# Kernel tuning notes

Measured on AMD Instinct MI355X. Metric: run time of the kernel, lower is better.

The kernel has to match this reference:

```python
import jax, jax.numpy as jnp
import numpy as np

NUM_HEADS = 16

def setup_inputs() -> dict:
    key = jax.random.key(0)
    k1, k2, k3, k4, k5 = jax.random.split(key, 5)
    B, N, C = 4, 2048, 1024
    N2, Cy = 1024, 768
    x = jax.random.normal(k1, (B, N, C), dtype=jnp.float32)
    y = jax.random.normal(k2, (B, N2, Cy), dtype=jnp.float32)
    pad_mask = jax.random.randint(k3, (B, N), 0, 2).astype(jnp.bool_)
    # Linear weights (torch convention: out = inp @ W.T), scaled ~ fan-in init
    Wq = jax.random.normal(k4, (C, C), dtype=jnp.float32) * (C ** -0.5)
    Wkv = jax.random.normal(k5, (2 * C, Cy), dtype=jnp.float32) * (Cy ** -0.5)
    return {"x": x, "y": y, "pad_mask": pad_mask, "Wq": Wq, "Wkv": Wkv}


def reference(x, y, pad_mask, Wq, Wkv):
    B, N, C = x.shape
    N2 = y.shape[1]
    H = NUM_HEADS
    d = C // H
    scale = d ** -0.5
    # q: [B, H, N, d]
    q = (x @ Wq.T).reshape(B, N, H, d).transpose(0, 2, 1, 3)
    # kv: [B, N2, 2, H, d] -> k, v each [B, H, N2, d]
    kv = (y @ Wkv.T).reshape(B, N2, 2, H, d).transpose(2, 0, 3, 1, 4)
    k, v = kv[0], kv[1]
    # scores: [B, H, N, N2]
    attn = jnp.einsum("bhnd,bhmd->bhnm", q * scale, k)
    # pad_mask is indexed by the QUERY axis and broadcast over keys (faithful
    # to the original einops.repeat 'B Q -> B H Q L'). False -> -1e9.
    attn = jnp.where(pad_mask[:, None, :, None], attn, jnp.float32(-1e9))
    attn = jax.nn.softmax(attn, axis=-1)
    out = jnp.einsum("bhnm,bhmd->bhnd", attn, v)  # [B, H, N, d]
    return out.transpose(0, 2, 1, 3).reshape(B, N, C)
```

## Files before the change

### kernel.cpp

```cpp
#include <hip/hip_runtime.h>

typedef unsigned short u16;
typedef unsigned int u32;
typedef __attribute__((ext_vector_type(8))) __bf16 bf16x8;
typedef __attribute__((ext_vector_type(4))) float f32x4;

__device__ __forceinline__ u16 f2bf(float f) {
  unsigned u = __float_as_uint(f);
  u += 0x7FFFu + ((u >> 16) & 1u);
  return (u16)(u >> 16);
}

__device__ __forceinline__ float fast_exp2(float x) { return __builtin_amdgcn_exp2f(x); }
__device__ __forceinline__ float fast_rcp(float x) { return __builtin_amdgcn_rcpf(x); }

__global__ void cvt_all(const float* __restrict__ x, const float* __restrict__ Wq,
                        const float* __restrict__ y, const float* __restrict__ Wkv,
                        const int* __restrict__ mask,
                        u16* __restrict__ Xb, u16* __restrict__ Wqb,
                        u16* __restrict__ Yb, u16* __restrict__ Wkvb) {
  int i = blockIdx.x * 256 + threadIdx.x;
  const float4* src;
  u16* dst;
  int j;
  float sc;
  if (i < 2097152) {
    j = i; src = (const float4*)x; dst = Xb;
    sc = (mask[i >> 8] != 0) ? 1.0f : 0.0f;
  } else if (i < 2359296) {
    j = i - 2097152; src = (const float4*)Wq; dst = Wqb;
    sc = 0.18033688f;
  } else if (i < 3145728) {
    j = i - 2359296; src = (const float4*)y; dst = Yb;
    sc = 1.0f;
  } else {
    j = i - 3145728; src = (const float4*)Wkv; dst = Wkvb;
    sc = 1.0f;
  }
  float4 v = src[j];
  ushort4 o;
  o.x = f2bf(v.x * sc);
  o.y = f2bf(v.y * sc);
  o.z = f2bf(v.z * sc);
  o.w = f2bf(v.w * sc);
  ((ushort4*)dst)[j] = o;
}

__global__ __launch_bounds__(256) void gemm_dual(
    const u16* __restrict__ Aq, const u16* __restrict__ Bq, u16* __restrict__ Cq,
    const u16* __restrict__ Akv, const u16* __restrict__ Bkv, u16* __restrict__ Ckv) {
  __shared__ __align__(16) u16 sA[2 * 128 * 32];
  __shared__ __align__(16) u16 sB[2 * 128 * 32];
  const int t = threadIdx.x;
  const int wave = t >> 6;
  const int lane = t & 63;
  const int wm = (wave >> 1) * 64;
  const int wn = (wave & 1) * 64;
  const int fr = lane & 15;
  const int quad = lane >> 4;
  const int fk = quad * 8;
  const int sr = lane >> 2;
  const int sc = (lane & 3) * 8;

  const u16 *A, *B;
  u16* C;
  int N, K, bx, by;
  const int blk = blockIdx.x;
  if (blk < 512) {
    A = Aq; B = Bq; C = Cq; N = 1024; K = 1024;
    by = blk >> 6; bx = blk & 63;
  } else {
    A = Akv; B = Bkv; C = Ckv; N = 2048; K = 768;
    const int id = blk - 512;
    by = id >> 5; bx = id & 31;
  }

  f32x4 acc[4][4];
  const f32x4 z4 = {0.f, 0.f, 0.f, 0.f};
#pragma unroll
  for (int i = 0; i < 4; ++i)
#pragma unroll
    for (int j = 0; j < 4; ++j) acc[i][j] = z4;

  const u16* Abase = A + (size_t)bx * 128 * K;
  const u16* Bbase = B + (size_t)by * 128 * K;

  auto stage = [&](int k0, u16* dA, u16* dB) {
#pragma unroll
    for (int q = 0; q < 2; ++q) {
      const int chunk = wave * 2 + q;
      const int row = chunk * 16 + sr;
      __builtin_amdgcn_global_load_lds(
          (__attribute__((address_space(1))) void*)(Abase + (size_t)row * K + k0 + sc),
          (__attribute__((address_space(3))) void*)(dA + chunk * 512), 16, 0, 0);
      __builtin_amdgcn_global_load_lds(
          (__attribute__((address_space(1))) void*)(Bbase + (size_t)row * K + k0 + sc),
          (__attribute__((address_space(3))) void*)(dB + chunk * 512), 16, 0, 0);
    }
  };

  stage(0, sA, sB);
  __syncthreads();

  int it = 0;
  for (int k0 = 0; k0 < K; k0 += 32, ++it) {
    u16* cA = sA + (it & 1) * 4096;
    u16* cB = sB + (it & 1) * 4096;
    if (k0 + 32 < K) stage(k0 + 32, sA + ((it + 1) & 1) * 4096, sB + ((it + 1) & 1) * 4096);

    bf16x8 af[4], bfv[4];
#pragma unroll
    for (int i = 0; i < 4; ++i)
      af[i] = *(const bf16x8*)(cA + (wm + i * 16 + fr) * 32 + fk);
#pragma unroll
    for (int j = 0; j < 4; ++j)
      bfv[j] = *(const bf16x8*)(cB + (wn + j * 16 + fr) * 32 + fk);
#pragma unroll
    for (int i = 0; i < 4; ++i)
#pragma unroll
      for (int j = 0; j < 4; ++j)
        acc[i][j] = __builtin_amdgcn_mfma_f32_16x16x32_bf16(af[i], bfv[j], acc[i][j], 0, 0, 0);

    if (k0 + 32 < K) __syncthreads();
  }

#pragma unroll
  for (int i = 0; i < 4; ++i)
#pragma unroll
    for (int j = 0; j < 4; ++j)
#pragma unroll
      for (int r = 0; r < 4; ++r) {
        const int row = bx * 128 + wm + i * 16 + quad * 4 + r;
        const int col = by * 128 + wn + j * 16 + fr;
        C[(size_t)row * N + col] = f2bf(acc[i][j][r]);
      }
}

__global__ void transpose_v(const u16* __restrict__ KV, u16* __restrict__ Vt) {
  __shared__ u16 tile[64][66];
  const int t = threadIdx.x;
  const int rb = blockIdx.x * 64;
  const int h = blockIdx.y;
#pragma unroll
  for (int i = 0; i < 16; ++i) {
    int idx = i * 256 + t;
    int r = idx >> 6, c = idx & 63;
    tile[r][c] = KV[(size_t)(rb + r) * 2048 + 1024 + h * 64 + c];
  }
  __syncthreads();
  const int b = blockIdx.x >> 4;
  const int n2b = (blockIdx.x & 15) * 64;
#pragma unroll
  for (int i = 0; i < 16; ++i) {
    int idx = i * 256 + t;
    int dd = idx >> 6, n2 = idx & 63;
    int cperm = (n2 & 32) | (((n2 >> 2) & 3) << 3) | (((n2 >> 4) & 1) << 2) | (n2 & 3);
    Vt[(size_t)((b * 16 + h) * 64 + dd) * 1024 + n2b + cperm] = tile[n2][dd];
  }
}

__global__ __launch_bounds__(256, 2) void attn_kernel(
    const u16* __restrict__ Q, const u16* __restrict__ KV,
    const u16* __restrict__ Vt, float* __restrict__ Out) {
  __shared__ __align__(16) u16 sK[2 * 128 * 64];
  __shared__ __align__(16) u16 sV[2 * 64 * 128];
  __shared__ float red[4][2][4][16];

  const int t = threadIdx.x;
  const int wave = t >> 6;
  const int lane = t & 63;
  const int g = blockIdx.x & 63;
  const int qt = blockIdx.x >> 6;
  const int b = g >> 4;
  const int h = g & 15;
  const int q0 = qt * 128;
  const int fr = lane & 15;
  const int quad = lane >> 4;
  const int l3 = lane >> 3, l7 = lane & 7;
  const int l4 = lane >> 4, l15 = lane & 15;

  const u16* qbase = Q + (size_t)(b * 2048 + q0 + wave * 16 + fr) * 1024 + h * 64 + quad * 8;
  bf16x8 qa[2][2];
  qa[0][0] = *(const bf16x8*)(qbase);
  qa[0][1] = *(const bf16x8*)(qbase + 32);
  qa[1][0] = *(const bf16x8*)(qbase + (size_t)64 * 1024);
  qa[1][1] = *(const bf16x8*)(qbase + (size_t)64 * 1024 + 32);

  const int kq = (l7 ^ l3) * 8;
  auto stage = [&](int kcn, u16* dK, u16* dV) {
#pragma unroll
    for (int i = 0; i < 4; ++i) {
      const int j = wave * 4 + i;
      const u16* ksrc = KV + (size_t)(b * 1024 + kcn * 128 + 8 * j + l3) * 2048 + h * 64 + kq;
      __builtin_amdgcn_global_load_lds(
          (__attribute__((address_space(1))) void*)ksrc,
          (__attribute__((address_space(3))) void*)(dK + j * 512), 16, 0, 0);
      const int vq = (l15 ^ ((i & 1) * 4 + l4)) * 8;
      const u16* vsrc = Vt + (size_t)((b * 16 + h) * 64 + 4 * j + l4) * 1024 + kcn * 128 + vq;
      __builtin_amdgcn_global_load_lds(
          (__attribute__((address_space(1))) void*)vsrc,
          (__attribute__((address_space(3))) void*)(dV + j * 512), 16, 0, 0);
    }
  };

  stage(0, sK, sV);
  __syncthreads();

  const f32x4 z4 = {0.f, 0.f, 0.f, 0.f};
  f32x4 o[2][4];
  float l_run[2] = {0.f, 0.f};
#pragma unroll
  for (int hh = 0; hh < 2; ++hh)
#pragma unroll
    for (int nt = 0; nt < 4; ++nt) o[hh][nt] = z4;

  const int f7 = fr & 7;
  const int ck0 = (quad ^ f7) * 8;
  const int ck1 = ((quad ^ 4) ^ f7) * 8;

  for (int kc = 0; kc < 8; ++kc) {
    const u16* sKc = sK + (kc & 1) * 8192;
    const u16* sVc = sV + (kc & 1) * 8192;
    if (kc < 7) stage(kc + 1, sK + ((kc + 1) & 1) * 8192, sV + ((kc + 1) & 1) * 8192);

#pragma unroll
    for (int ks = 0; ks < 4; ++ks) {
      f32x4 s0[2], s1[2];
      {
        const u16* kb = sKc + ((2 * ks) * 16 + fr) * 64;
        bf16x8 k0 = *(const bf16x8*)(kb + ck0);
        bf16x8 k1 = *(const bf16x8*)(kb + ck1);
        s0[0] = __builtin_amdgcn_mfma_f32_16x16x32_bf16(k0, qa[0][0], z4, 0, 0, 0);
        s0[0] = __builtin_amdgcn_mfma_f32_16x16x32_bf16(k1, qa[0][1], s0[0], 0, 0, 0);
        s0[1] = __builtin_amdgcn_mfma_f32_16x16x32_bf16(k0, qa[1][0], z4, 0, 0, 0);
        s0[1] = __builtin_amdgcn_mfma_f32_16x16x32_bf16(k1, qa[1][1], s0[1], 0, 0, 0);
      }
      {
        const u16* kb = sKc + ((2 * ks + 1) * 16 + fr) * 64;
        bf16x8 k0 = *(const bf16x8*)(kb + ck0);
        bf16x8 k1 = *(const bf16x8*)(kb + ck1);
        s1[0] = __builtin_amdgcn_mfma_f32_16x16x32_bf16(k0, qa[0][0], z4, 0, 0, 0);
        s1[0] = __builtin_amdgcn_mfma_f32_16x16x32_bf16(k1, qa[0][1], s1[0], 0, 0, 0);
        s1[1] = __builtin_amdgcn_mfma_f32_16x16x32_bf16(k0, qa[1][0], z4, 0, 0, 0);
        s1[1] = __builtin_amdgcn_mfma_f32_16x16x32_bf16(k1, qa[1][1], s1[1], 0, 0, 0);
      }

      bf16x8 pa[2];
#pragma unroll
      for (int hh = 0; hh < 2; ++hh) {
        f32x4& a = (hh == 0) ? s0[0] : s0[1];
        f32x4& bb = (hh == 0) ? s1[0] : s1[1];
        float l = 0.f;
#pragma unroll
        for (int r = 0; r < 4; ++r) {
          float p0 = fast_exp2(a[r]); a[r] = p0; l += p0;
          float p1 = fast_exp2(bb[r]); bb[r] = p1; l += p1;
        }
        l_run[hh] += l;
        bf16x8 pv;
        pv[0] = (__bf16)a[0];  pv[1] = (__bf16)a[1];
        pv[2] = (__bf16)a[2];  pv[3] = (__bf16)a[3];
        pv[4] = (__bf16)bb[0]; pv[5] = (__bf16)bb[1];
        pv[6] = (__bf16)bb[2]; pv[7] = (__bf16)bb[3];
        pa[hh] = pv;
      }

#pragma unroll
      for (int ntd = 0; ntd < 4; ++ntd) {
        const int cv = (((ks * 4 + quad) ^ f7)) * 8;
        bf16x8 vb = *(const bf16x8*)(sVc + (ntd * 16 + fr) * 128 + cv);
        o[0][ntd] = __builtin_amdgcn_mfma_f32_16x16x32_bf16(pa[0], vb, o[0][ntd], 0, 0, 0);
        o[1][ntd] = __builtin_amdgcn_mfma_f32_16x16x32_bf16(pa[1], vb, o[1][ntd], 0, 0, 0);
      }
    }

    if (kc < 7) __syncthreads();
  }

  red[wave][0][quad][fr] = l_run[0];
  red[wave][1][quad][fr] = l_run[1];
  __syncthreads();

#pragma unroll
  for (int hh = 0; hh < 2; ++hh) {
    float inv[4];
#pragma unroll
    for (int r = 0; r < 4; ++r) {
      const int ql = quad * 4 + r;
      float d = red[wave][hh][0][ql] + red[wave][hh][1][ql] +
                red[wave][hh][2][ql] + red[wave][hh][3][ql];
      inv[r] = fast_rcp(d);
    }
#pragma unroll
    for (int ntd = 0; ntd < 4; ++ntd)
#pragma unroll
      for (int r = 0; r < 4; ++r) {
        const int row = q0 + hh * 64 + wave * 16 + quad * 4 + r;
        const int col = h * 64 + ntd * 16 + fr;
        Out[(size_t)(b * 2048 + row) * 1024 + col] = o[hh][ntd][r] * inv[r];
      }
  }
}

extern "C" void kernel_launch(void* const* d_in, const int* in_sizes, int n_in,
                              void* d_out, int out_size, void* d_ws, size_t ws_size,
                              hipStream_t stream) {
  (void)in_sizes; (void)n_in; (void)out_size; (void)ws_size;
  const float* x   = (const float*)d_in[0];
  const float* y   = (const float*)d_in[1];
  const int*   msk = (const int*)d_in[2];
  const float* Wq  = (const float*)d_in[3];
  const float* Wkv = (const float*)d_in[4];
  float* out = (float*)d_out;

  char* ws = (char*)d_ws;
  const size_t MB = 1024 * 1024;
  u16* Xb   = (u16*)(ws + 0);
  u16* Wqb  = (u16*)(ws + 16 * MB);
  u16* Yb   = (u16*)(ws + 18 * MB);
  u16* Wkvb = (u16*)(ws + 24 * MB);
  u16* Qb   = (u16*)(ws + 27 * MB);
  u16* KVb  = (u16*)(ws + 43 * MB);
  u16* Vtb  = (u16*)(ws + 59 * MB);

  cvt_all<<<13824, 256, 0, stream>>>(x, Wq, y, Wkv, msk, Xb, Wqb, Yb, Wkvb);
  gemm_dual<<<1024, 256, 0, stream>>>(Xb, Wqb, Qb, Yb, Wkvb, KVb);
  transpose_v<<<dim3(64, 16), 256, 0, stream>>>(KVb, Vtb);
  attn_kernel<<<1024, 256, 0, stream>>>(Qb, KVb, Vtb, out);
}
```

Baseline: 189.8 us.

## Fuse V transpose into KV GEMM epilogue and unroll conversion kernel

The separate transpose_v kernel is removed. GEMM blocks that produce the V half of KV now stage their tile through shared memory and write the permuted transposed V layout directly, which saves one launch and a full read/write pass over V. The bf16 conversion kernel now handles four float4 per thread with a quarter of the blocks. The trade-offs are a larger shared allocation, extra syncs in the GEMM epilogue, and the fact that V is no longer written to the KV buffer itself, which is fine only if attention reads V solely from Vt.

New measurement: 180.5 us. 1.05x faster.

```diff
diff --git a/kernel.cpp b/kernel.cpp
--- a/kernel.cpp
+++ b/kernel.cpp
@@ -19,38 +19,45 @@
                         const int* __restrict__ mask,
                         u16* __restrict__ Xb, u16* __restrict__ Wqb,
                         u16* __restrict__ Yb, u16* __restrict__ Wkvb) {
-  int i = blockIdx.x * 256 + threadIdx.x;
+  const int t = threadIdx.x;
+  const int blk = blockIdx.x;
   const float4* src;
   u16* dst;
-  int j;
+  int jb;
   float sc;
-  if (i < 2097152) {
-    j = i; src = (const float4*)x; dst = Xb;
-    sc = (mask[i >> 8] != 0) ? 1.0f : 0.0f;
-  } else if (i < 2359296) {
-    j = i - 2097152; src = (const float4*)Wq; dst = Wqb;
+  bool m0 = false;
+  if (blk < 2048) {
+    src = (const float4*)x; dst = Xb; jb = blk * 1024 + t; m0 = true; sc = 1.0f;
+  } else if (blk < 2304) {
+    src = (const float4*)Wq; dst = Wqb; jb = (blk - 2048) * 1024 + t;
     sc = 0.18033688f;
-  } else if (i < 3145728) {
-    j = i - 2359296; src = (const float4*)y; dst = Yb;
-    sc = 1.0f;
+  } else if (blk < 3072) {
+    src = (const float4*)y; dst = Yb; jb = (blk - 2304) * 1024 + t; sc = 1.0f;
   } else {
-    j = i - 3145728; src = (const float4*)Wkv; dst = Wkvb;
-    sc = 1.0f;
-  }
-  float4 v = src[j];
-  ushort4 o;
-  o.x = f2bf(v.x * sc);
-  o.y = f2bf(v.y * sc);
-  o.z = f2bf(v.z * sc);
-  o.w = f2bf(v.w * sc);
-  ((ushort4*)dst)[j] = o;
+    src = (const float4*)Wkv; dst = Wkvb; jb = (blk - 3072) * 1024 + t; sc = 1.0f;
+  }
+#pragma unroll
+  for (int u = 0; u < 4; ++u) {
+    const int j = jb + u * 256;
+    float s = sc;
+    if (m0) s = (mask[j >> 8] != 0) ? 1.0f : 0.0f;
+    float4 v = src[j];
+    ushort4 o;
+    o.x = f2bf(v.x * s);
+    o.y = f2bf(v.y * s);
+    o.z = f2bf(v.z * s);
+    o.w = f2bf(v.w * s);
+    ((ushort4*)dst)[j] = o;
+  }
 }
 
 __global__ __launch_bounds__(256) void gemm_dual(
     const u16* __restrict__ Aq, const u16* __restrict__ Bq, u16* __restrict__ Cq,
-    const u16* __restrict__ Akv, const u16* __restrict__ Bkv, u16* __restrict__ Ckv) {
-  __shared__ __align__(16) u16 sA[2 * 128 * 32];
-  __shared__ __align__(16) u16 sB[2 * 128 * 32];
+    const u16* __restrict__ Akv, const u16* __restrict__ Bkv, u16* __restrict__ Ckv,
+    u16* __restrict__ Vt) {
+  __shared__ __align__(16) u16 smem[17408];
+  u16* sA = smem;
+  u16* sB = smem + 8192;
   const int t = threadIdx.x;
   const int wave = t >> 6;
   const int lane = t & 63;
@@ -124,38 +131,46 @@
     if (k0 + 32 < K) __syncthreads();
   }
 
-#pragma unroll
-  for (int i = 0; i < 4; ++i)
-#pragma unroll
-    for (int j = 0; j < 4; ++j)
-#pragma unroll
-      for (int r = 0; r < 4; ++r) {
-        const int row = bx * 128 + wm + i * 16 + quad * 4 + r;
-        const int col = by * 128 + wn + j * 16 + fr;
-        C[(size_t)row * N + col] = f2bf(acc[i][j][r]);
-      }
-}
-
-__global__ void transpose_v(const u16* __restrict__ KV, u16* __restrict__ Vt) {
-  __shared__ u16 tile[64][66];
-  const int t = threadIdx.x;
-  const int rb = blockIdx.x * 64;
-  const int h = blockIdx.y;
-#pragma unroll
-  for (int i = 0; i < 16; ++i) {
-    int idx = i * 256 + t;
-    int r = idx >> 6, c = idx & 63;
-    tile[r][c] = KV[(size_t)(rb + r) * 2048 + 1024 + h * 64 + c];
-  }
-  __syncthreads();
-  const int b = blockIdx.x >> 4;
-  const int n2b = (blockIdx.x & 15) * 64;
-#pragma unroll
-  for (int i = 0; i < 16; ++i) {
-    int idx = i * 256 + t;
-    int dd = idx >> 6, n2 = idx & 63;
-    int cperm = (n2 & 32) | (((n2 >> 2) & 3) << 3) | (((n2 >> 4) & 1) << 2) | (n2 & 3);
-    Vt[(size_t)((b * 16 + h) * 64 + dd) * 1024 + n2b + cperm] = tile[n2][dd];
+  if (blk >= 512 && by >= 8) {
+    __syncthreads();
+#pragma unroll
+    for (int i = 0; i < 4; ++i)
+#pragma unroll
+      for (int j = 0; j < 4; ++j) {
+        ushort4 o;
+        o.x = f2bf(acc[i][j][0]);
+        o.y = f2bf(acc[i][j][1]);
+        o.z = f2bf(acc[i][j][2]);
+        o.w = f2bf(acc[i][j][3]);
+        *(ushort4*)(smem + (wn + j * 16 + fr) * 136 + wm + i * 16 + quad * 4) = o;
+      }
+    __syncthreads();
+    const int b = bx >> 3;
+#pragma unroll
+    for (int i2 = 0; i2 < 32; ++i2) {
+      const int flat = i2 * 256 + t;
+      const int hdl = flat >> 6;
+      const int pp = flat & 63;
+      const int gg = pp >> 5;
+      const int pe = (pp & 31) * 2;
+      const int m = (pe & 32) | (pe & 3) | (((pe >> 3) & 3) << 2) | (((pe >> 2) & 1) << 4);
+      const u32 val = *(const u32*)(smem + hdl * 136 + gg * 64 + m);
+      const int h = (by - 8) * 2 + (hdl >> 6);
+      const int dd = hdl & 63;
+      *(u32*)(Vt + (size_t)((b * 16 + h) * 64 + dd) * 1024 +
+              (bx & 7) * 128 + gg * 64 + pe) = val;
+    }
+  } else {
+#pragma unroll
+    for (int i = 0; i < 4; ++i)
+#pragma unroll
+      for (int j = 0; j < 4; ++j)
+#pragma unroll
+        for (int r = 0; r < 4; ++r) {
+          const int row = bx * 128 + wm + i * 16 + quad * 4 + r;
+          const int col = by * 128 + wn + j * 16 + fr;
+          C[(size_t)row * N + col] = f2bf(acc[i][j][r]);
+        }
   }
 }
 
@@ -323,8 +338,7 @@
   u16* KVb  = (u16*)(ws + 43 * MB);
   u16* Vtb  = (u16*)(ws + 59 * MB);
 
-  cvt_all<<<13824, 256, 0, stream>>>(x, Wq, y, Wkv, msk, Xb, Wqb, Yb, Wkvb);
-  gemm_dual<<<1024, 256, 0, stream>>>(Xb, Wqb, Qb, Yb, Wkvb, KVb);
-  transpose_v<<<dim3(64, 16), 256, 0, stream>>>(KVb, Vtb);
+  cvt_all<<<3456, 256, 0, stream>>>(x, Wq, y, Wkv, msk, Xb, Wqb, Yb, Wkvb);
+  gemm_dual<<<1024, 256, 0, stream>>>(Xb, Wqb, Qb, Yb, Wkvb, KVb, Vtb);
   attn_kernel<<<1024, 256, 0, stream>>>(Qb, KVb, Vtb, out);
 }
```
